# Performance work log

Measured on AMD Instinct MI355X. Metric: run time of the kernel, lower is better.

Reference implementation:

```python
import jax, jax.numpy as jnp
import numpy as np

H = 16        # num_attention_heads
HS = 128      # head_size
ROT = 32      # rotary_ndims (partial RoPE, NeoX rotary_pct=0.25)
BASE = 10000.0


def _rope_cache(seq_len):
    inv_freq = 1.0 / (BASE ** (jnp.arange(0, ROT, 2, dtype=jnp.float32) / ROT))
    t = jnp.arange(seq_len, dtype=jnp.float32)
    freqs = jnp.outer(t, inv_freq)                      # [s, ROT/2]
    emb = jnp.concatenate([freqs, freqs], axis=-1)      # [s, ROT]
    return jnp.cos(emb), jnp.sin(emb)


def _rotate_half(x):
    x1, x2 = jnp.split(x, 2, axis=-1)
    return jnp.concatenate([-x2, x1], axis=-1)


def setup_inputs() -> dict:
    key = jax.random.key(0)
    k1, k2, k3 = jax.random.split(key, 3)
    B, S, D = 2, 2048, 2048
    hidden_states = jax.random.normal(k1, (B, S, D), dtype=jnp.float32)
    position_ids = jnp.broadcast_to(jnp.arange(S, dtype=jnp.int64 if jax.config.jax_enable_x64 else jnp.int32), (B, S))
    W_qkv = jax.random.normal(k2, (D, 3 * H * HS), dtype=jnp.float32) * 0.02
    b_qkv = jnp.zeros((3 * H * HS,), dtype=jnp.float32)
    W_dense = jax.random.normal(k3, (H * HS, D), dtype=jnp.float32) * 0.02
    b_dense = jnp.zeros((D,), dtype=jnp.float32)
    return {"hidden_states": hidden_states, "position_ids": position_ids,
            "W_qkv": W_qkv, "b_qkv": b_qkv, "W_dense": W_dense, "b_dense": b_dense}


def reference(hidden_states, position_ids, W_qkv, b_qkv, W_dense, b_dense):
    B, S, D = hidden_states.shape
    # fused QKV projection, NeoX layout: [b, s, h, 3*hs]
    qkv = (hidden_states @ W_qkv + b_qkv).reshape(B, S, H, 3 * HS)
    q = qkv[..., :HS]            # [b, s, h, hs]
    k = qkv[..., HS:2 * HS]
    v = qkv[..., 2 * HS:]

    # partial rotary embedding on first ROT dims
    cos, sin = _rope_cache(S)                       # [s, ROT]
    cos = cos[position_ids][:, :, None, :]          # [b, s, 1, ROT]
    sin = sin[position_ids][:, :, None, :]
    q_rot, q_pass = q[..., :ROT], q[..., ROT:]
    k_rot, k_pass = k[..., :ROT], k[..., ROT:]
    q_rot = q_rot * cos + _rotate_half(q_rot) * sin
    k_rot = k_rot * cos + _rotate_half(k_rot) * sin
    q = jnp.concatenate([q_rot, q_pass], axis=-1)
    k = jnp.concatenate([k_rot, k_pass], axis=-1)

    # scaled dot-product attention (no mask, as in the source SDPA call)
    scale = 1.0 / jnp.sqrt(jnp.asarray(HS, dtype=q.dtype))
    scores = jnp.einsum('bqhd,bkhd->bhqk', q, k) * scale   # [b, h, s, s]
    attn = jax.nn.softmax(scores, axis=-1)
    out = jnp.einsum('bhqk,bkhd->bqhd', attn, v)            # [b, s, h, hs]
    out = out.reshape(B, S, H * HS)                         # 'b h d n -> b d (h n)'
    return out @ W_dense + b_dense
```

## Files before the change

kernel.cpp:

```cpp
#include <hip/hip_runtime.h>

typedef short bf16x8 __attribute__((ext_vector_type(8)));
typedef float f32x4 __attribute__((ext_vector_type(4)));

#define S_LEN 2048
#define NHEAD 16
#define HSZ 128

__device__ __forceinline__ float bf2f(ushort u) {
    union { unsigned int i; float f; } x; x.i = ((unsigned int)u) << 16; return x.f;
}
__device__ __forceinline__ ushort f2bf(float f) {
    union { float f; unsigned int i; } x; x.f = f;
    unsigned int r = (x.i + 0x7FFFu + ((x.i >> 16) & 1u)) >> 16;
    return (ushort)r;
}

__device__ __forceinline__ void gload16(const ushort* g, ushort* l) {
    __builtin_amdgcn_global_load_lds(
        (const __attribute__((address_space(1))) unsigned int*)g,
        (__attribute__((address_space(3))) unsigned int*)l,
        16, 0, 0);
}

#define BAR()   asm volatile("s_barrier" ::: "memory")
#define LGKM0() asm volatile("s_waitcnt lgkmcnt(0)" ::: "memory")

__device__ __forceinline__ void transpose_body(
    const float* __restrict__ W, ushort* __restrict__ WT,
    int K, int N, int bx, int by, float (*tile)[33]) {
    int tx = threadIdx.x & 31, ty = threadIdx.x >> 5;
    int n = bx * 32 + tx;
    #pragma unroll
    for (int j = 0; j < 32; j += 8) {
        int k = by * 32 + ty + j;
        tile[ty + j][tx] = W[(size_t)k * N + n];
    }
    __syncthreads();
    int k2 = by * 32 + tx;
    #pragma unroll
    for (int j = 0; j < 32; j += 8) {
        int n2 = bx * 32 + ty + j;
        WT[(size_t)n2 * K + k2] = f2bf(tile[tx][ty + j]);
    }
}

__global__ __launch_bounds__(256) void prep_kernel(
    const float* __restrict__ hidden, ushort* __restrict__ hA,
    const float* __restrict__ Wqkv, ushort* __restrict__ WqT,
    const float* __restrict__ Wd, ushort* __restrict__ WdT) {
    __shared__ float tile[32][33];
    int bid = blockIdx.x;
    if (bid < 8192) {
        int i = bid * 256 + threadIdx.x;
        float4 v = ((const float4*)hidden)[i];
        ushort4 r;
        r.x = f2bf(v.x); r.y = f2bf(v.y); r.z = f2bf(v.z); r.w = f2bf(v.w);
        ((ushort4*)hA)[i] = r;
    } else if (bid < 8192 + 12288) {
        int tb = bid - 8192;
        transpose_body(Wqkv, WqT, 2048, 6144, tb % 192, tb / 192, tile);
    } else {
        int tb = bid - 20480;
        transpose_body(Wd, WdT, 2048, 2048, tb % 64, tb / 64, tile);
    }
}

template <int EPI>
__global__ __launch_bounds__(512, 2) void gemm256(
    const ushort* __restrict__ A, const ushort* __restrict__ Bt,
    const float* __restrict__ bias, float* __restrict__ Cout, int Kdim, int Ndim,
    ushort* __restrict__ q_out, ushort* __restrict__ k_out, ushort* __restrict__ v_out,
    const int* __restrict__ pos_ids) {
    __shared__ __align__(16) ushort lds[65536];
    const int tid = threadIdx.x;
    const int m0 = blockIdx.y * 256, n0 = blockIdx.x * 256;
    const int lane = tid & 63, wid = tid >> 6;
    const int wm = wid >> 2, wn = wid & 3;
    const int lm = lane & 15, quad = lane >> 4;
    const int cs = (quad ^ ((lm >> 1) & 3)) * 8;
    const int aOff = wm * 8192 + lm * 32 + cs;
    const int bOff = 16384 + (wn >> 1) * 8192 + (wn & 1) * 2048 + lm * 32 + cs;
    const int srow = tid >> 2;
    const int xs8 = ((tid & 3) ^ ((tid >> 3) & 3)) * 8;
    const ushort* pAs = A  + (size_t)(m0 + srow) * Kdim + xs8;
    const ushort* pBs = Bt + (size_t)(n0 + srow) * Kdim + xs8;
    const size_t hK = (size_t)128 * Kdim;
    const int sw = wid * 512;

    f32x4 acc[8][4];
    #pragma unroll
    for (int i = 0; i < 8; ++i)
        #pragma unroll
        for (int j = 0; j < 4; ++j) acc[i][j] = (f32x4){0.f, 0.f, 0.f, 0.f};

    const int T = Kdim >> 6;

    auto stageB = [&](int t) {
        ushort* b = lds + (t & 1) * 32768 + 16384 + sw;
        const ushort* g = pBs + (size_t)t * 64;
        gload16(g,            b);
        gload16(g + 32,       b + 4096);
        gload16(g + hK,       b + 8192);
        gload16(g + hK + 32,  b + 12288);
    };
    auto stageA = [&](int t) {
        ushort* b = lds + (t & 1) * 32768 + sw;
        const ushort* g = pAs + (size_t)t * 64;
        gload16(g,            b);
        gload16(g + 32,       b + 4096);
        gload16(g + hK,       b + 8192);
        gload16(g + hK + 32,  b + 12288);
    };

    stageB(0); stageA(0); stageB(1); stageA(1);
    asm volatile("s_waitcnt vmcnt(8)" ::: "memory");
    BAR();

    bf16x8 afC[8], bfC[4], afN[8], bfN[4];
    #pragma unroll
    for (int mt = 0; mt < 8; ++mt) afC[mt] = *(const bf16x8*)(lds + aOff + mt * 512);
    #pragma unroll
    for (int nt = 0; nt < 4; ++nt) bfC[nt] = *(const bf16x8*)(lds + bOff + nt * 512);

    for (int t = 0; t < T; ++t) {
        const ushort* la = lds + (t & 1) * 32768 + aOff;
        const ushort* lb = lds + (t & 1) * 32768 + bOff;
        const bool pf = (t + 2 < T);

        #pragma unroll
        for (int mt = 0; mt < 8; ++mt) afN[mt] = *(const bf16x8*)(la + 4096 + mt * 512);
        #pragma unroll
        for (int nt = 0; nt < 4; ++nt) bfN[nt] = *(const bf16x8*)(lb + 4096 + nt * 512);
        __builtin_amdgcn_s_setprio(1);
        #pragma unroll
        for (int mt = 0; mt < 8; ++mt)
            #pragma unroll
            for (int nt = 0; nt < 4; ++nt)
                acc[mt][nt] = __builtin_amdgcn_mfma_f32_16x16x32_bf16(
                    afC[mt], bfC[nt], acc[mt][nt], 0, 0, 0);
        __builtin_amdgcn_s_setprio(0);
        LGKM0();
        BAR();

        if (pf) { stageB(t + 2); stageA(t + 2); }
        __builtin_amdgcn_s_setprio(1);
        #pragma unroll
        for (int mt = 0; mt < 8; ++mt)
            #pragma unroll
            for (int nt = 0; nt < 4; ++nt)
                acc[mt][nt] = __builtin_amdgcn_mfma_f32_16x16x32_bf16(
                    afN[mt], bfN[nt], acc[mt][nt], 0, 0, 0);
        __builtin_amdgcn_s_setprio(0);
        if (pf) asm volatile("s_waitcnt vmcnt(8)" ::: "memory");
        else    asm volatile("s_waitcnt vmcnt(0)" ::: "memory");
        BAR();

        if (t + 1 < T) {
            const ushort* la2 = lds + ((t + 1) & 1) * 32768 + aOff;
            const ushort* lb2 = lds + ((t + 1) & 1) * 32768 + bOff;
            #pragma unroll
            for (int mt = 0; mt < 8; ++mt) afC[mt] = *(const bf16x8*)(la2 + mt * 512);
            #pragma unroll
            for (int nt = 0; nt < 4; ++nt) bfC[nt] = *(const bf16x8*)(lb2 + nt * 512);
        }
    }

    if (EPI == 0) {
        const int woff = (n0 + wn * 64) % 384;
        const int rot = (woff == 0 || woff == 128) ? 1 : 0;
        float invf = 0.f;
        if (rot) invf = exp2f(-(float)lm * 0.8304820237218405f);
        const int gnb = n0 + wn * 64 + lm;
        #pragma unroll
        for (int mt = 0; mt < 8; ++mt) {
            f32x4 w[4];
            #pragma unroll
            for (int nt = 0; nt < 4; ++nt) {
                float bv = bias[gnb + nt * 16];
                #pragma unroll
                for (int i = 0; i < 4; ++i) w[nt][i] = acc[mt][nt][i] + bv;
            }
            if (rot) {
                #pragma unroll
                for (int i = 0; i < 4; ++i) {
                    int gm = m0 + wm * 128 + mt * 16 + quad * 4 + i;
                    int bI = gm >> 11, s = gm & 2047;
                    float th = (float)pos_ids[bI * S_LEN + s] * invf;
                    float sf, cf;
                    sincosf(th, &sf, &cf);
                    float x1 = w[0][i], x2 = w[1][i];
                    w[0][i] = x1 * cf - x2 * sf;
                    w[1][i] = x2 * cf + x1 * sf;
                }
            }
            #pragma unroll
            for (int nt = 0; nt < 4; ++nt) {
                int gn = gnb + nt * 16;
                int h = gn / 384, r = gn - h * 384;
                int tt = r >> 7, d = r & 127;
                #pragma unroll
                for (int i = 0; i < 4; ++i) {
                    int gm = m0 + wm * 128 + mt * 16 + quad * 4 + i;
                    int b = gm >> 11, s = gm & 2047;
                    ushort bb = f2bf(w[nt][i]);
                    if (tt == 0) {
                        q_out[((size_t)(b * NHEAD + h) * S_LEN + s) * HSZ + d] = bb;
                    } else if (tt == 1) {
                        k_out[((size_t)(b * NHEAD + h) * S_LEN + s) * HSZ + d] = bb;
                    } else {
                        v_out[((size_t)(b * NHEAD + h) * HSZ + d) * S_LEN + s] = bb;
                    }
                }
            }
        }
    } else {
        #pragma unroll
        for (int mt = 0; mt < 8; ++mt) {
            #pragma unroll
            for (int nt = 0; nt < 4; ++nt) {
                f32x4 c = acc[mt][nt];
                int gn = n0 + wn * 64 + nt * 16 + lm;
                float bv = bias[gn];
                #pragma unroll
                for (int i = 0; i < 4; ++i) {
                    int gm = m0 + wm * 128 + mt * 16 + quad * 4 + i;
                    Cout[(size_t)gm * Ndim + gn] = c[i] + bv;
                }
            }
        }
    }
}

template <int EPI>
__global__ __launch_bounds__(256) void gemm128(
    const ushort* __restrict__ A, const ushort* __restrict__ Bt,
    const float* __restrict__ bias, float* __restrict__ Cout, int Kdim, int Ndim,
    ushort* __restrict__ q_out, ushort* __restrict__ k_out, ushort* __restrict__ v_out) {
    __shared__ __align__(16) ushort lA[2][128 * 32];
    __shared__ __align__(16) ushort lB[2][128 * 32];
    const int tid = threadIdx.x;
    const int m0 = blockIdx.y * 128, n0 = blockIdx.x * 128;
    const int lane = tid & 63, wid = tid >> 6;
    const int wm = wid >> 1, wn = wid & 1, lm = lane & 15, quad = lane >> 4;
    const int srow = tid >> 2;
    const int gc = (tid & 3) ^ ((tid >> 3) & 3);
    const int wb8 = (wid << 6) * 8;
    const int cs = (quad ^ ((lm >> 1) & 3)) * 8;

    const ushort* pA = A  + (size_t)(m0 + srow) * Kdim + gc * 8;
    const ushort* pB = Bt + (size_t)(n0 + srow) * Kdim + gc * 8;
    const size_t rhalf = (size_t)64 * Kdim;

    const int fA = (wm * 64 + lm) * 32;
    const int fB = (wn * 64 + lm) * 32;

    f32x4 acc[16];
    #pragma unroll
    for (int i = 0; i < 16; ++i) acc[i] = (f32x4){0.f, 0.f, 0.f, 0.f};

    const int T = Kdim >> 5;
    gload16(pA,         lA[0] + wb8);
    gload16(pA + rhalf, lA[0] + 2048 + wb8);
    gload16(pB,         lB[0] + wb8);
    gload16(pB + rhalf, lB[0] + 2048 + wb8);
    pA += 32; pB += 32;

    for (int t = 0; t < T; ++t) {
        __syncthreads();
        const ushort* la = lA[t & 1];
        const ushort* lb = lB[t & 1];
        if (t + 1 < T) {
            ushort* da = lA[(t + 1) & 1];
            ushort* db = lB[(t + 1) & 1];
            gload16(pA,         da + wb8);
            gload16(pA + rhalf, da + 2048 + wb8);
            gload16(pB,         db + wb8);
            gload16(pB + rhalf, db + 2048 + wb8);
            pA += 32; pB += 32;
        }
        bf16x8 af[4], bfr[4];
        #pragma unroll
        for (int t4 = 0; t4 < 4; ++t4) {
            af[t4]  = *(const bf16x8*)(la + fA + t4 * 512 + cs);
            bfr[t4] = *(const bf16x8*)(lb + fB + t4 * 512 + cs);
        }
        #pragma unroll
        for (int mt = 0; mt < 4; ++mt)
            #pragma unroll
            for (int nt = 0; nt < 4; ++nt)
                acc[mt * 4 + nt] = __builtin_amdgcn_mfma_f32_16x16x32_bf16(
                    af[mt], bfr[nt], acc[mt * 4 + nt], 0, 0, 0);
    }

    #pragma unroll
    for (int mt = 0; mt < 4; ++mt) {
        #pragma unroll
        for (int nt = 0; nt < 4; ++nt) {
            f32x4 c = acc[mt * 4 + nt];
            int gn = n0 + wn * 64 + nt * 16 + lm;
            float bv = bias[gn];
            #pragma unroll
            for (int i = 0; i < 4; ++i) {
                int gm = m0 + wm * 64 + mt * 16 + quad * 4 + i;
                float v = c[i] + bv;
                if (EPI == 0) {
                    int h = gn / 384, r = gn - h * 384;
                    int t = r >> 7, d = r & 127;
                    int b = gm >> 11, s = gm & 2047;
                    ushort bb = f2bf(v);
                    if (t == 0) {
                        q_out[((size_t)(b * NHEAD + h) * S_LEN + s) * HSZ + d] = bb;
                    } else if (t == 1) {
                        k_out[((size_t)(b * NHEAD + h) * S_LEN + s) * HSZ + d] = bb;
                    } else {
                        v_out[((size_t)(b * NHEAD + h) * HSZ + d) * S_LEN + s] = bb;
                    }
                } else {
                    Cout[(size_t)gm * Ndim + gn] = v;
                }
            }
        }
    }
}

__global__ __launch_bounds__(512, 2) void attn_mfma(
    const ushort* __restrict__ Q, const ushort* __restrict__ K,
    const ushort* __restrict__ Vt, ushort* __restrict__ O) {
    __shared__ __align__(16) ushort lQ[256 * 136];
    __shared__ __align__(16) ushort lK[2][64 * 128];
    __shared__ __align__(16) ushort lVt[2][128 * 64];
    __shared__ __align__(16) ushort lP[8 * 32 * 40];

    const int tid = threadIdx.x;
    const int wid = tid >> 6, lane = tid & 63;
    const int L = lane & 15, quad = lane >> 4;
    const int bid0 = blockIdx.y * 8 + blockIdx.x;
    const int swz = (bid0 & 7) * 32 + (bid0 >> 3);
    const int bh = swz >> 3;
    const int q0 = (swz & 7) * 256;
    const int wq0 = wid * 32;
    const size_t base = (size_t)bh * S_LEN * HSZ;
    const ushort* Qb = Q + base + (size_t)q0 * HSZ;
    const ushort* Kb = K + base;
    const ushort* Vb = Vt + base;
    ushort* lPw = lP + wid * (32 * 40);

    #pragma unroll
    for (int p = 0; p < 8; ++p) {
        int idx = tid + p * 512;
        int row = idx >> 4, ch = idx & 15;
        uint4 v = ((const uint4*)Qb)[idx];
        *(uint4*)(lQ + row * 136 + ch * 8) = v;
    }
    __syncthreads();

    bf16x8 qf[2][4];
    #pragma unroll
    for (int qs = 0; qs < 2; ++qs)
        #pragma unroll
        for (int dc = 0; dc < 4; ++dc)
            qf[qs][dc] = *(const bf16x8*)(lQ + (wq0 + qs * 16 + L) * 136 + dc * 32 + quad * 8);

    int kx[4];
    #pragma unroll
    for (int dc = 0; dc < 4; ++dc) kx[dc] = ((dc * 4 + quad) ^ (L & 7)) * 8;
    const int vx0 = ((0 * 4 + quad) ^ (L & 7)) * 8;
    const int vx1 = ((1 * 4 + quad) ^ (L & 7)) * 8;

    const int ub  = (tid & 0x1C0) * 8;
    const int kr0 = tid >> 4,  kg0 = (tid & 15) ^ (kr0 & 7);
    const int kr1 = kr0 + 32;
    const int vd0 = tid >> 3,  vg0 = (tid & 7) ^ (vd0 & 7);
    const int vd1 = vd0 + 64;

    f32x4 acc_o[8][2];
    #pragma unroll
    for (int dt = 0; dt < 8; ++dt)
        #pragma unroll
        for (int qs = 0; qs < 2; ++qs) acc_o[dt][qs] = (f32x4){0.f, 0.f, 0.f, 0.f};
    float lacc[2] = {0.f, 0.f};
    const float scale = 0.08838834764831845f;
    const float SHIFT = 12.0f;

    {
        gload16(Kb + (size_t)kr0 * 128 + kg0 * 8, lK[0] + ub);
        gload16(Kb + (size_t)kr1 * 128 + kg0 * 8, lK[0] + 4096 + ub);
        gload16(Vb + (size_t)vd0 * 2048 + vg0 * 8, lVt[0] + ub);
        gload16(Vb + (size_t)vd1 * 2048 + vg0 * 8, lVt[0] + 4096 + ub);
    }

    for (int kt = 0; kt < S_LEN / 64; ++kt) {
        __syncthreads();
        const int cur = kt & 1;
        const ushort* lKc = lK[cur];
        const ushort* lVc = lVt[cur];
        if (kt + 1 < S_LEN / 64) {
            ushort* dK = lK[cur ^ 1];
            ushort* dV = lVt[cur ^ 1];
            int kb = (kt + 1) * 64;
            gload16(Kb + (size_t)(kb + kr0) * 128 + kg0 * 8, dK + ub);
            gload16(Kb + (size_t)(kb + kr1) * 128 + kg0 * 8, dK + 4096 + ub);
            gload16(Vb + (size_t)vd0 * 2048 + kb + vg0 * 8, dV + ub);
            gload16(Vb + (size_t)vd1 * 2048 + kb + vg0 * 8, dV + 4096 + ub);
        }

        f32x4 sa[4][2];
        #pragma unroll
        for (int t = 0; t < 4; ++t)
            #pragma unroll
            for (int qs = 0; qs < 2; ++qs) sa[t][qs] = (f32x4){0.f, 0.f, 0.f, 0.f};
        #pragma unroll
        for (int t = 0; t < 4; ++t)
            #pragma unroll
            for (int dc = 0; dc < 4; ++dc) {
                bf16x8 kf = *(const bf16x8*)(lKc + (t * 16 + L) * 128 + kx[dc]);
                sa[t][0] = __builtin_amdgcn_mfma_f32_16x16x32_bf16(kf, qf[0][dc], sa[t][0], 0, 0, 0);
                sa[t][1] = __builtin_amdgcn_mfma_f32_16x16x32_bf16(kf, qf[1][dc], sa[t][1], 0, 0, 0);
            }

        #pragma unroll
        for (int h = 0; h < 2; ++h) {
            #pragma unroll
            for (int t2 = 0; t2 < 2; ++t2) {
                int t = h * 2 + t2;
                #pragma unroll
                for (int qs = 0; qs < 2; ++qs) {
                    #pragma unroll
                    for (int r = 0; r < 4; ++r) {
                        float pv = __expf(fmaf(sa[t][qs][r], scale, -SHIFT));
                        lacc[qs] += pv;
                        sa[t][qs][r] = pv;
                    }
                    ushort4 u;
                    u.x = f2bf(sa[t][qs][0]);
                    u.y = f2bf(sa[t][qs][1]);
                    u.z = f2bf(sa[t][qs][2]);
                    u.w = f2bf(sa[t][qs][3]);
                    *(ushort4*)(lPw + (qs * 16 + L) * 40 + t2 * 16 + quad * 4) = u;
                }
            }
            LGKM0();
            bf16x8 pf0 = *(const bf16x8*)(lPw + L * 40 + quad * 8);
            bf16x8 pf1 = *(const bf16x8*)(lPw + (16 + L) * 40 + quad * 8);
            const int vx = h ? vx1 : vx0;
            #pragma unroll
            for (int dt = 0; dt < 8; ++dt) {
                bf16x8 vf = *(const bf16x8*)(lVc + (dt * 16 + L) * 64 + vx);
                acc_o[dt][0] = __builtin_amdgcn_mfma_f32_16x16x32_bf16(vf, pf0, acc_o[dt][0], 0, 0, 0);
                acc_o[dt][1] = __builtin_amdgcn_mfma_f32_16x16x32_bf16(vf, pf1, acc_o[dt][1], 0, 0, 0);
            }
        }
    }

    const int b = bh >> 4, h = bh & 15;
    #pragma unroll
    for (int qs = 0; qs < 2; ++qs) {
        float l = lacc[qs];
        l += __shfl_xor(l, 16);
        l += __shfl_xor(l, 32);
        float inv = 1.f / l;
        size_t row = ((size_t)(b * S_LEN + q0 + wq0 + qs * 16 + L)) * (NHEAD * HSZ) + h * HSZ;
        #pragma unroll
        for (int dt = 0; dt < 8; ++dt) {
            ushort4 u;
            u.x = f2bf(acc_o[dt][qs][0] * inv);
            u.y = f2bf(acc_o[dt][qs][1] * inv);
            u.z = f2bf(acc_o[dt][qs][2] * inv);
            u.w = f2bf(acc_o[dt][qs][3] * inv);
            *(ushort4*)(O + row + dt * 16 + quad * 4) = u;
        }
    }
}

extern "C" void kernel_launch(void* const* d_in, const int* in_sizes, int n_in,
                              void* d_out, int out_size, void* d_ws, size_t ws_size,
                              hipStream_t stream) {
    const float* hidden = (const float*)d_in[0];
    const int*   pos    = (const int*)d_in[1];
    const float* Wqkv   = (const float*)d_in[2];
    const float* bqkv   = (const float*)d_in[3];
    const float* Wd     = (const float*)d_in[4];
    const float* bd     = (const float*)d_in[5];

    char* ws = (char*)d_ws;
    ushort* hA  = (ushort*)ws;
    ushort* WqT = (ushort*)(ws + 16777216ull);
    ushort* WdT = (ushort*)(ws + 41943040ull);
    ushort* Qb  = (ushort*)(ws + 50331648ull);
    ushort* Kb  = (ushort*)(ws + 67108864ull);
    ushort* Vb  = (ushort*)(ws + 83886080ull);

    prep_kernel<<<dim3(24576), dim3(256), 0, stream>>>(hidden, hA, Wqkv, WqT, Wd, WdT);

    gemm256<0><<<dim3(24, 16), dim3(512), 0, stream>>>(hA, WqT, bqkv, nullptr, 2048, 6144,
                                                       Qb, Kb, Vb, pos);

    ushort* Obuf = hA;
    attn_mfma<<<dim3(8, 32), dim3(512), 0, stream>>>(Qb, Kb, Vb, Obuf);

    gemm128<1><<<dim3(16, 32), dim3(256), 0, stream>>>(Obuf, WdT, bd, (float*)d_out,
                                                       2048, 2048, nullptr, nullptr, nullptr);
}
```

Measured before the change: 416.7 us.

## Double attention KV tile to 128, load Q directly, vectorize V-transpose stores

The attention kernel now stages 128-key K and V tiles per iteration instead of 64, halving the number of loop iterations and barriers, and loads Q fragments straight from global memory, dropping the LDS Q staging buffer and its barrier. The QKV GEMM epilogue hoists row index math and writes the transposed V output as 4-element vector stores instead of scalar stores. The larger K/V buffers raise LDS use to about 148 KB per block, which may limit occupancy against the launch bound of 2 blocks. Direct Q loads are uncoalesced per lane.

```diff
diff --git a/kernel.cpp b/kernel.cpp
--- a/kernel.cpp
+++ b/kernel.cpp
@@ -181,12 +181,12 @@
                 #pragma unroll
                 for (int i = 0; i < 4; ++i) w[nt][i] = acc[mt][nt][i] + bv;
             }
+            const int gm0 = m0 + wm * 128 + mt * 16 + quad * 4;
+            const int b0 = gm0 >> 11, s0 = gm0 & 2047;
             if (rot) {
                 #pragma unroll
                 for (int i = 0; i < 4; ++i) {
-                    int gm = m0 + wm * 128 + mt * 16 + quad * 4 + i;
-                    int bI = gm >> 11, s = gm & 2047;
-                    float th = (float)pos_ids[bI * S_LEN + s] * invf;
+                    float th = (float)pos_ids[b0 * S_LEN + s0 + i] * invf;
                     float sf, cf;
                     sincosf(th, &sf, &cf);
                     float x1 = w[0][i], x2 = w[1][i];
@@ -199,18 +199,16 @@
                 int gn = gnb + nt * 16;
                 int h = gn / 384, r = gn - h * 384;
                 int tt = r >> 7, d = r & 127;
-                #pragma unroll
-                for (int i = 0; i < 4; ++i) {
-                    int gm = m0 + wm * 128 + mt * 16 + quad * 4 + i;
-                    int b = gm >> 11, s = gm & 2047;
-                    ushort bb = f2bf(w[nt][i]);
-                    if (tt == 0) {
-                        q_out[((size_t)(b * NHEAD + h) * S_LEN + s) * HSZ + d] = bb;
-                    } else if (tt == 1) {
-                        k_out[((size_t)(b * NHEAD + h) * S_LEN + s) * HSZ + d] = bb;
-                    } else {
-                        v_out[((size_t)(b * NHEAD + h) * HSZ + d) * S_LEN + s] = bb;
-                    }
+                if (tt == 2) {
+                    ushort4 u;
+                    u.x = f2bf(w[nt][0]); u.y = f2bf(w[nt][1]);
+                    u.z = f2bf(w[nt][2]); u.w = f2bf(w[nt][3]);
+                    *(ushort4*)(v_out + ((size_t)(b0 * NHEAD + h) * HSZ + d) * S_LEN + s0) = u;
+                } else {
+                    ushort* dst = (tt == 0) ? q_out : k_out;
+                    #pragma unroll
+                    for (int i = 0; i < 4; ++i)
+                        dst[((size_t)(b0 * NHEAD + h) * S_LEN + s0 + i) * HSZ + d] = f2bf(w[nt][i]);
                 }
             }
         }
@@ -327,9 +325,8 @@
 __global__ __launch_bounds__(512, 2) void attn_mfma(
     const ushort* __restrict__ Q, const ushort* __restrict__ K,
     const ushort* __restrict__ Vt, ushort* __restrict__ O) {
-    __shared__ __align__(16) ushort lQ[256 * 136];
-    __shared__ __align__(16) ushort lK[2][64 * 128];
-    __shared__ __align__(16) ushort lVt[2][128 * 64];
+    __shared__ __align__(16) ushort lK[2][128 * 128];
+    __shared__ __align__(16) ushort lVt[2][128 * 128];
     __shared__ __align__(16) ushort lP[8 * 32 * 40];
 
     const int tid = threadIdx.x;
@@ -346,33 +343,21 @@
     const ushort* Vb = Vt + base;
     ushort* lPw = lP + wid * (32 * 40);
 
-    #pragma unroll
-    for (int p = 0; p < 8; ++p) {
-        int idx = tid + p * 512;
-        int row = idx >> 4, ch = idx & 15;
-        uint4 v = ((const uint4*)Qb)[idx];
-        *(uint4*)(lQ + row * 136 + ch * 8) = v;
-    }
-    __syncthreads();
-
     bf16x8 qf[2][4];
     #pragma unroll
     for (int qs = 0; qs < 2; ++qs)
         #pragma unroll
         for (int dc = 0; dc < 4; ++dc)
-            qf[qs][dc] = *(const bf16x8*)(lQ + (wq0 + qs * 16 + L) * 136 + dc * 32 + quad * 8);
+            qf[qs][dc] = *(const bf16x8*)(Qb + (size_t)(wq0 + qs * 16 + L) * HSZ
+                                          + dc * 32 + quad * 8);
 
     int kx[4];
     #pragma unroll
     for (int dc = 0; dc < 4; ++dc) kx[dc] = ((dc * 4 + quad) ^ (L & 7)) * 8;
-    const int vx0 = ((0 * 4 + quad) ^ (L & 7)) * 8;
-    const int vx1 = ((1 * 4 + quad) ^ (L & 7)) * 8;
-
-    const int ub  = (tid & 0x1C0) * 8;
-    const int kr0 = tid >> 4,  kg0 = (tid & 15) ^ (kr0 & 7);
-    const int kr1 = kr0 + 32;
-    const int vd0 = tid >> 3,  vg0 = (tid & 7) ^ (vd0 & 7);
-    const int vd1 = vd0 + 64;
+
+    const int sr = tid >> 4;
+    const int sg = (tid & 15) ^ (sr & 7);
+    const int ub = (tid & 0x1C0) * 8;
 
     f32x4 acc_o[8][2];
     #pragma unroll
@@ -383,35 +368,37 @@
     const float scale = 0.08838834764831845f;
     const float SHIFT = 12.0f;
 
-    {
-        gload16(Kb + (size_t)kr0 * 128 + kg0 * 8, lK[0] + ub);
-        gload16(Kb + (size_t)kr1 * 128 + kg0 * 8, lK[0] + 4096 + ub);
-        gload16(Vb + (size_t)vd0 * 2048 + vg0 * 8, lVt[0] + ub);
-        gload16(Vb + (size_t)vd1 * 2048 + vg0 * 8, lVt[0] + 4096 + ub);
-    }
-
-    for (int kt = 0; kt < S_LEN / 64; ++kt) {
+    #pragma unroll
+    for (int l = 0; l < 4; ++l) {
+        int r = sr + l * 32;
+        gload16(Kb + (size_t)r * 128 + sg * 8,  lK[0]  + ub + l * 4096);
+        gload16(Vb + (size_t)r * 2048 + sg * 8, lVt[0] + ub + l * 4096);
+    }
+
+    for (int kt = 0; kt < S_LEN / 128; ++kt) {
         __syncthreads();
         const int cur = kt & 1;
         const ushort* lKc = lK[cur];
         const ushort* lVc = lVt[cur];
-        if (kt + 1 < S_LEN / 64) {
+        if (kt + 1 < S_LEN / 128) {
             ushort* dK = lK[cur ^ 1];
             ushort* dV = lVt[cur ^ 1];
-            int kb = (kt + 1) * 64;
-            gload16(Kb + (size_t)(kb + kr0) * 128 + kg0 * 8, dK + ub);
-            gload16(Kb + (size_t)(kb + kr1) * 128 + kg0 * 8, dK + 4096 + ub);
-            gload16(Vb + (size_t)vd0 * 2048 + kb + vg0 * 8, dV + ub);
-            gload16(Vb + (size_t)vd1 * 2048 + kb + vg0 * 8, dV + 4096 + ub);
-        }
-
-        f32x4 sa[4][2];
-        #pragma unroll
-        for (int t = 0; t < 4; ++t)
+            int kb = (kt + 1) * 128;
+            #pragma unroll
+            for (int l = 0; l < 4; ++l) {
+                int r = sr + l * 32;
+                gload16(Kb + (size_t)(kb + r) * 128 + sg * 8,      dK + ub + l * 4096);
+                gload16(Vb + (size_t)r * 2048 + kb + sg * 8,       dV + ub + l * 4096);
+            }
+        }
+
+        f32x4 sa[8][2];
+        #pragma unroll
+        for (int t = 0; t < 8; ++t)
             #pragma unroll
             for (int qs = 0; qs < 2; ++qs) sa[t][qs] = (f32x4){0.f, 0.f, 0.f, 0.f};
         #pragma unroll
-        for (int t = 0; t < 4; ++t)
+        for (int t = 0; t < 8; ++t)
             #pragma unroll
             for (int dc = 0; dc < 4; ++dc) {
                 bf16x8 kf = *(const bf16x8*)(lKc + (t * 16 + L) * 128 + kx[dc]);
@@ -420,7 +407,7 @@
             }
 
         #pragma unroll
-        for (int h = 0; h < 2; ++h) {
+        for (int h = 0; h < 4; ++h) {
             #pragma unroll
             for (int t2 = 0; t2 < 2; ++t2) {
                 int t = h * 2 + t2;
@@ -443,10 +430,10 @@
             LGKM0();
             bf16x8 pf0 = *(const bf16x8*)(lPw + L * 40 + quad * 8);
             bf16x8 pf1 = *(const bf16x8*)(lPw + (16 + L) * 40 + quad * 8);
-            const int vx = h ? vx1 : vx0;
+            const int vx = ((h * 4 + quad) ^ (L & 7)) * 8;
             #pragma unroll
             for (int dt = 0; dt < 8; ++dt) {
-                bf16x8 vf = *(const bf16x8*)(lVc + (dt * 16 + L) * 64 + vx);
+                bf16x8 vf = *(const bf16x8*)(lVc + (dt * 16 + L) * 128 + vx);
                 acc_o[dt][0] = __builtin_amdgcn_mfma_f32_16x16x32_bf16(vf, pf0, acc_o[dt][0], 0, 0, 0);
                 acc_o[dt][1] = __builtin_amdgcn_mfma_f32_16x16x32_bf16(vf, pf1, acc_o[dt][1], 0, 0, 0);
             }
```

New measurement: 406.9 us. 2.3% less time.
